# Optimization experiments

Measured on AMD Instinct MI355X. Metric: run time of the kernel, lower is better.

## Reference

```python
import jax, jax.numpy as jnp
import numpy as np

T = 0.1  # temperature (init arg t)


def setup_inputs() -> dict:
    key = jax.random.key(0)
    k0, k1, k2, k3 = jax.random.split(key, 4)
    B, C, H, W, N = 1, 64, 256, 256, 4096
    emb_0 = jax.random.normal(k0, (B, C, H, W), dtype=jnp.float32)
    emb_1 = jax.random.normal(k1, (B, C, H, W), dtype=jnp.float32)
    # module assumes embeddings are already L2-normalized along channels
    emb_0 = emb_0 / jnp.linalg.norm(emb_0, axis=1, keepdims=True)
    emb_1 = emb_1 / jnp.linalg.norm(emb_1, axis=1, keepdims=True)
    locations_0 = jax.random.randint(k2, (B, N, 2), 0, H).astype(jnp.float32)
    locations_1 = jax.random.randint(k3, (B, N, 2), 0, H).astype(jnp.float32)
    return {"emb_0": emb_0, "emb_1": emb_1,
            "locations_0": locations_0, "locations_1": locations_1}


def reference(emb_0, emb_1, locations_0, locations_1):
    b, c, H, W = emb_0.shape  # b == 1
    n = locations_0.shape[1]
    v = H * W
    # (b, v, c)
    e0 = emb_0.reshape(b, c, v).transpose(0, 2, 1)
    e1 = emb_1.reshape(b, c, v).transpose(0, 2, 1)
    # flatten 2D coords to linear indices: strides [W, 1]
    ind_kernel = jnp.array([W, 1], dtype=jnp.float32)
    ind_0 = (jnp.floor(locations_0) @ ind_kernel).astype(jnp.int32)[0]  # (n,)
    ind_1 = (jnp.floor(locations_1) @ ind_kernel).astype(jnp.int32)[0]  # (n,)
    e0 = e0[:, ind_0, :]  # (b, n, c)
    e1 = e1[:, ind_1, :]  # (b, n, c)
    emb = jnp.concatenate([e0, e1], axis=1)  # (b, 2n, c)
    sim = jnp.einsum('bic,bjc->bij', emb, emb)  # (b, 2n, 2n)
    exp = jnp.exp(sim / T)
    sum_e = jnp.sum(exp, axis=2) - np.exp(1.0 / T)  # subtract self-similarity
    u = jnp.arange(n)
    w = u + n
    e_uv = exp[:, u, w]  # (b, n) positive pairs
    loss = -jnp.sum(jnp.log(e_uv / sum_e[:, u]) + jnp.log(e_uv / sum_e[:, w]))
    return loss / (2 * n)
```

## Files before the change

kernel.cpp:

```cpp
#include <hip/hip_runtime.h>
#include <math.h>

#define HW2     65536
#define NLOC    4096
#define NROW    8192
#define CDIM    64
#define TINV    10.0f
#define EXP10   22026.465794806718f
#define NP      64
#define NPAIR   2080

#if __has_builtin(__builtin_amdgcn_exp2f)
#define ASCALE  14.426950408889634f
#define EXPFN(x) __builtin_amdgcn_exp2f(x)
#else
#define ASCALE  10.0f
#define EXPFN(x) __expf(x)
#endif

typedef __attribute__((ext_vector_type(8))) short bf16x8;
typedef __attribute__((ext_vector_type(4))) float f32x4;
typedef unsigned short u16;

__device__ __forceinline__ unsigned short f2bf(float f) {
  unsigned u = __builtin_bit_cast(unsigned, f);
  u += 0x7FFFu + ((u >> 16) & 1u);
  return (unsigned short)(u >> 16);
}
__device__ __forceinline__ float bf2f(unsigned u16v) {
  unsigned u = u16v << 16;
  return __builtin_bit_cast(float, u);
}
__device__ __forceinline__ bf16x8 scale8(bf16x8 r) {
  bf16x8 o;
#pragma unroll
  for (int j = 0; j < 8; ++j)
    o[j] = (short)f2bf(bf2f((unsigned short)r[j]) * ASCALE);
  return o;
}

__global__ __launch_bounds__(256) void gatherc_kernel(
    const float* __restrict__ emb0, const float* __restrict__ emb1,
    const float* __restrict__ loc0, const float* __restrict__ loc1,
    u16* __restrict__ Gb, unsigned* __restrict__ counter) {
  __shared__ int ind[64];
  __shared__ u16 Gs[64][18];

  const int tid   = threadIdx.x;
  const int chunk = blockIdx.x;
  const int cg    = blockIdx.y;
  const int eb    = chunk >> 6;
  const float* emb = eb ? emb1 : emb0;
  const float* loc = eb ? loc1 : loc0;

  if (chunk == 0 && cg == 0 && tid == 0) *counter = 0u;

  if (tid < 64) {
    const int u = (chunk & 63) * 64 + tid;
    float2 lv = *reinterpret_cast<const float2*>(&loc[u * 2]);
    ind[tid] = (int)floorf(lv.x) * 256 + (int)floorf(lv.y);
  }
  __syncthreads();

  const int row = tid & 63;
  const int cq  = tid >> 6;
  const int pos = ind[row];
#pragma unroll
  for (int k = 0; k < 4; ++k) {
    const int cl = cq + 4 * k;
    float v = emb[(size_t)(cg * 16 + cl) * HW2 + pos];
    Gs[row][cl] = f2bf(v);
  }
  __syncthreads();

  if (tid < 128) {
    const int r2 = tid >> 1, h = tid & 1;
    bf16x8 v = *reinterpret_cast<const bf16x8*>(&Gs[r2][h * 8]);
    *reinterpret_cast<bf16x8*>(
        &Gb[(size_t)(chunk * 64 + r2) * CDIM + cg * 16 + h * 8]) = v;
  }
}

__device__ __forceinline__ void stage_tile(u16* Bs, const u16* __restrict__ Gb,
                                           int jb, int buf, int tid, int wave,
                                           int srow, int ssl) {
#pragma unroll
  for (int r = 0; r < 2; ++r) {
    const u16* src = Gb + (size_t)(jb + r * 32 + srow) * CDIM + ssl * 8;
#if __has_builtin(__builtin_amdgcn_global_load_lds)
    u16* dst = Bs + buf * 4096 + r * 2048 + wave * 512;
    __builtin_amdgcn_global_load_lds(
        (const __attribute__((address_space(1))) unsigned int*)src,
        (__attribute__((address_space(3))) unsigned int*)dst, 16, 0, 0);
#else
    bf16x8 tmp = *reinterpret_cast<const bf16x8*>(src);
    *reinterpret_cast<bf16x8*>(Bs + buf * 4096 + r * 2048 + tid * 8) = tmp;
#endif
  }
}

__global__ __launch_bounds__(256) void simsum_tri_kernel(
    const u16* __restrict__ Gb, float* __restrict__ rowPart) {
  __shared__ u16 Bs[2 * 64 * CDIM];
  __shared__ float colRed[4][128];

  const int tid  = threadIdx.x;
  const int lane = tid & 63;
  const int wave = tid >> 6;
  const int lrow = lane & 15;
  const int kh   = lane >> 4;

  const int b = blockIdx.x;
  int p = (int)((129.0f - sqrtf(16641.0f - 8.0f * (float)b)) * 0.5f);
  if (p < 0) p = 0;
  if (p > NP - 1) p = NP - 1;
#pragma unroll
  for (int it = 0; it < 3; ++it) {
    if (p > 0 && (p * NP - p * (p - 1) / 2) > b) --p;
    else if (((p + 1) * NP - (p + 1) * p / 2) <= b) ++p;
  }
  const int q  = p + (b - (p * NP - p * (p - 1) / 2));
  const int p0 = p * 128, q0 = q * 128;
  const int i0 = p0 + wave * 32;

  const bf16x8* arowA =
      reinterpret_cast<const bf16x8*>(Gb + (size_t)(i0 + lrow) * CDIM + kh * 8);
  const bf16x8* arowB = reinterpret_cast<const bf16x8*>(
      Gb + (size_t)(i0 + 16 + lrow) * CDIM + kh * 8);
  bf16x8 aA0 = scale8(arowA[0]), aA1 = scale8(arowA[4]);
  bf16x8 aB0 = scale8(arowB[0]), aB1 = scale8(arowB[4]);

  const int srow = tid >> 3;
  const int ssl  = (tid & 7) ^ (srow & 7);
  stage_tile(Bs, Gb, q0,      0, tid, wave, srow, ssl);
  stage_tile(Bs, Gb, q0 + 64, 1, tid, wave, srow, ssl);
  __syncthreads();

  const int sp0 = ((kh ^ (lrow & 7)) << 3);
  const int sp1 = (((4 + kh) ^ (lrow & 7)) << 3);

  float accA[4][4], accB[4][4];
#pragma unroll
  for (int nf = 0; nf < 4; ++nf)
#pragma unroll
    for (int r = 0; r < 4; ++r) { accA[nf][r] = 0.f; accB[nf][r] = 0.f; }
  float colAcc[2][4];

#pragma unroll
  for (int t = 0; t < 2; ++t) {
    const u16* bs = Bs + t * 4096;
#pragma unroll
    for (int nf = 0; nf < 4; ++nf) {
      const int rb = (nf * 16 + lrow) * CDIM;
      bf16x8 b0 = *reinterpret_cast<const bf16x8*>(bs + rb + sp0);
      bf16x8 b1 = *reinterpret_cast<const bf16x8*>(bs + rb + sp1);
      f32x4 z = {0.f, 0.f, 0.f, 0.f};
      f32x4 tA = __builtin_amdgcn_mfma_f32_16x16x32_bf16(aA0, b0, z, 0, 0, 0);
      tA = __builtin_amdgcn_mfma_f32_16x16x32_bf16(aA1, b1, tA, 0, 0, 0);
      f32x4 tB = __builtin_amdgcn_mfma_f32_16x16x32_bf16(aB0, b0, z, 0, 0, 0);
      tB = __builtin_amdgcn_mfma_f32_16x16x32_bf16(aB1, b1, tB, 0, 0, 0);
      float cp = 0.f;
#pragma unroll
      for (int r = 0; r < 4; ++r) {
        float eA = EXPFN(tA[r]);
        float eB = EXPFN(tB[r]);
        accA[nf][r] += eA;
        accB[nf][r] += eB;
        cp += eA + eB;
      }
      colAcc[t][nf] = cp;
    }
  }

#pragma unroll
  for (int r = 0; r < 4; ++r) {
    float vA = (accA[0][r] + accA[1][r]) + (accA[2][r] + accA[3][r]);
    float vB = (accB[0][r] + accB[1][r]) + (accB[2][r] + accB[3][r]);
    vA += __shfl_xor(vA, 1, 16);
    vA += __shfl_xor(vA, 2, 16);
    vA += __shfl_xor(vA, 4, 16);
    vA += __shfl_xor(vA, 8, 16);
    vB += __shfl_xor(vB, 1, 16);
    vB += __shfl_xor(vB, 2, 16);
    vB += __shfl_xor(vB, 4, 16);
    vB += __shfl_xor(vB, 8, 16);
    if (lrow == 0) {
      rowPart[(size_t)(i0 + kh * 4 + r) * NP + q] = vA;
      rowPart[(size_t)(i0 + 16 + kh * 4 + r) * NP + q] = vB;
    }
  }

  if (p != q) {
#pragma unroll
    for (int t = 0; t < 2; ++t)
#pragma unroll
      for (int nf = 0; nf < 4; ++nf) {
        float c = colAcc[t][nf];
        c += __shfl_xor(c, 16, 64);
        c += __shfl_xor(c, 32, 64);
        if (kh == 0) colRed[wave][t * 64 + nf * 16 + lrow] = c;
      }
    __syncthreads();
    if (tid < 128) {
      float s = (colRed[0][tid] + colRed[1][tid]) +
                (colRed[2][tid] + colRed[3][tid]);
      rowPart[(size_t)(q0 + tid) * NP + p] = s;
    }
  }
}

__global__ __launch_bounds__(256) void finpart_kernel(
    const u16* __restrict__ Gb, const float* __restrict__ rowPart,
    float* __restrict__ partA, float* __restrict__ partB,
    unsigned* __restrict__ counter, float* __restrict__ out) {
  __shared__ float sA[256];
  __shared__ float sB[256];
  __shared__ int lastFlag;
  const int tid = threadIdx.x, b = blockIdx.x;

  float logAcc = 0.f;
  if (tid < 128) {
    const int row = b * 128 + tid;
    const float4* rp = reinterpret_cast<const float4*>(rowPart + (size_t)row * NP);
    float s = 0.f;
#pragma unroll
    for (int c = 0; c < NP / 4; ++c) {
      float4 v = rp[c];
      s += (v.x + v.y) + (v.z + v.w);
    }
    logAcc = logf(s - EXP10);
  }
  float cross = 0.f;
  if (tid < 64) {
    const int u = b * 64 + tid;
    const unsigned* r0 = reinterpret_cast<const unsigned*>(Gb + (size_t)u * CDIM);
    const unsigned* r1 =
        reinterpret_cast<const unsigned*>(Gb + (size_t)(u + NLOC) * CDIM);
#pragma unroll
    for (int c = 0; c < 32; ++c) {
      unsigned a = r0[c], bb = r1[c];
      cross += bf2f(a & 0xffffu) * bf2f(bb & 0xffffu) + bf2f(a >> 16) * bf2f(bb >> 16);
    }
  }
  sA[tid] = logAcc;
  sB[tid] = cross;
  __syncthreads();
  for (int s = 128; s > 0; s >>= 1) {
    if (tid < s) { sA[tid] += sA[tid + s]; sB[tid] += sB[tid + s]; }
    __syncthreads();
  }
  if (tid == 0) {
    __hip_atomic_store(&partA[b], sA[0], __ATOMIC_RELAXED, __HIP_MEMORY_SCOPE_AGENT);
    __hip_atomic_store(&partB[b], sB[0], __ATOMIC_RELAXED, __HIP_MEMORY_SCOPE_AGENT);
    __threadfence();
    unsigned old = atomicAdd(counter, 1u);
    lastFlag = (old == 63u) ? 1 : 0;
  }
  __syncthreads();

  if (lastFlag && tid < 64) {
    float a = __hip_atomic_load(&partA[tid], __ATOMIC_RELAXED, __HIP_MEMORY_SCOPE_AGENT);
    float c = __hip_atomic_load(&partB[tid], __ATOMIC_RELAXED, __HIP_MEMORY_SCOPE_AGENT);
#pragma unroll
    for (int s = 1; s < 64; s <<= 1) {
      a += __shfl_xor(a, s, 64);
      c += __shfl_xor(c, s, 64);
    }
    if (tid == 0) out[0] = (a - 2.0f * TINV * c) / (float)NROW;
  }
}

extern "C" void kernel_launch(void* const* d_in, const int* in_sizes, int n_in,
                              void* d_out, int out_size, void* d_ws, size_t ws_size,
                              hipStream_t stream) {
  const float* emb0 = (const float*)d_in[0];
  const float* emb1 = (const float*)d_in[1];
  const float* loc0 = (const float*)d_in[2];
  const float* loc1 = (const float*)d_in[3];
  float* out = (float*)d_out;
  char* ws = (char*)d_ws;

  u16* Gb           = (u16*)ws;
  float* rowPart    = (float*)(ws + (1ull << 20));
  float* partA      = (float*)(ws + (3ull << 20));
  float* partB      = (float*)(ws + (3ull << 20) + 256);
  unsigned* counter = (unsigned*)(ws + (3ull << 20) + 512);

  dim3 gg(128, 4);
  gatherc_kernel<<<gg, 256, 0, stream>>>(emb0, emb1, loc0, loc1, Gb, counter);
  simsum_tri_kernel<<<NPAIR, 256, 0, stream>>>(Gb, rowPart);
  finpart_kernel<<<64, 256, 0, stream>>>(Gb, rowPart, partA, partB, counter, out);
}
```

Measured before the change: 37.28 us.

## Make triangular sim kernel loop over tiles with double-buffered LDS prefetch

The similarity-sum kernel now launches a fixed 1024 blocks. Each block walks the triangular tile list with stride SBLK, and while it computes the current tile it prefetches the next tile's B operand into a second LDS buffer. The goal is to hide global-to-LDS staging latency and cut per-block launch and setup overhead. In exchange the LDS footprint doubles, which may lower occupancy. Because 2080 tiles do not divide evenly over 1024 blocks, some blocks take a third tile and leave an uneven tail.

```diff
diff --git a/kernel.cpp b/kernel.cpp
--- a/kernel.cpp
+++ b/kernel.cpp
@@ -9,6 +9,7 @@
 #define EXP10   22026.465794806718f
 #define NP      64
 #define NPAIR   2080
+#define SBLK    1024
 
 #if __has_builtin(__builtin_amdgcn_exp2f)
 #define ASCALE  14.426950408889634f
@@ -39,6 +40,19 @@
   return o;
 }
 
+__device__ __forceinline__ void tri_decode(int b, int* pOut, int* qOut) {
+  int p = (int)((129.0f - sqrtf(16641.0f - 8.0f * (float)b)) * 0.5f);
+  if (p < 0) p = 0;
+  if (p > NP - 1) p = NP - 1;
+#pragma unroll
+  for (int it = 0; it < 3; ++it) {
+    if (p > 0 && (p * NP - p * (p - 1) / 2) > b) --p;
+    else if (((p + 1) * NP - (p + 1) * p / 2) <= b) ++p;
+  }
+  *pOut = p;
+  *qOut = p + (b - (p * NP - p * (p - 1) / 2));
+}
+
 __global__ __launch_bounds__(256) void gatherc_kernel(
     const float* __restrict__ emb0, const float* __restrict__ emb1,
     const float* __restrict__ loc0, const float* __restrict__ loc1,
@@ -81,27 +95,27 @@
   }
 }
 
-__device__ __forceinline__ void stage_tile(u16* Bs, const u16* __restrict__ Gb,
-                                           int jb, int buf, int tid, int wave,
+__device__ __forceinline__ void stage_tile(u16* base, const u16* __restrict__ Gb,
+                                           int jb, int half, int tid, int wave,
                                            int srow, int ssl) {
 #pragma unroll
   for (int r = 0; r < 2; ++r) {
     const u16* src = Gb + (size_t)(jb + r * 32 + srow) * CDIM + ssl * 8;
 #if __has_builtin(__builtin_amdgcn_global_load_lds)
-    u16* dst = Bs + buf * 4096 + r * 2048 + wave * 512;
+    u16* dst = base + half * 4096 + r * 2048 + wave * 512;
     __builtin_amdgcn_global_load_lds(
         (const __attribute__((address_space(1))) unsigned int*)src,
         (__attribute__((address_space(3))) unsigned int*)dst, 16, 0, 0);
 #else
     bf16x8 tmp = *reinterpret_cast<const bf16x8*>(src);
-    *reinterpret_cast<bf16x8*>(Bs + buf * 4096 + r * 2048 + tid * 8) = tmp;
+    *reinterpret_cast<bf16x8*>(base + half * 4096 + r * 2048 + tid * 8) = tmp;
 #endif
   }
 }
 
 __global__ __launch_bounds__(256) void simsum_tri_kernel(
     const u16* __restrict__ Gb, float* __restrict__ rowPart) {
-  __shared__ u16 Bs[2 * 64 * CDIM];
+  __shared__ u16 Bs[2][2 * 64 * CDIM];
   __shared__ float colRed[4][128];
 
   const int tid  = threadIdx.x;
@@ -109,103 +123,115 @@
   const int wave = tid >> 6;
   const int lrow = lane & 15;
   const int kh   = lane >> 4;
-
-  const int b = blockIdx.x;
-  int p = (int)((129.0f - sqrtf(16641.0f - 8.0f * (float)b)) * 0.5f);
-  if (p < 0) p = 0;
-  if (p > NP - 1) p = NP - 1;
-#pragma unroll
-  for (int it = 0; it < 3; ++it) {
-    if (p > 0 && (p * NP - p * (p - 1) / 2) > b) --p;
-    else if (((p + 1) * NP - (p + 1) * p / 2) <= b) ++p;
-  }
-  const int q  = p + (b - (p * NP - p * (p - 1) / 2));
-  const int p0 = p * 128, q0 = q * 128;
-  const int i0 = p0 + wave * 32;
-
-  const bf16x8* arowA =
-      reinterpret_cast<const bf16x8*>(Gb + (size_t)(i0 + lrow) * CDIM + kh * 8);
-  const bf16x8* arowB = reinterpret_cast<const bf16x8*>(
-      Gb + (size_t)(i0 + 16 + lrow) * CDIM + kh * 8);
-  bf16x8 aA0 = scale8(arowA[0]), aA1 = scale8(arowA[4]);
-  bf16x8 aB0 = scale8(arowB[0]), aB1 = scale8(arowB[4]);
-
   const int srow = tid >> 3;
   const int ssl  = (tid & 7) ^ (srow & 7);
-  stage_tile(Bs, Gb, q0,      0, tid, wave, srow, ssl);
-  stage_tile(Bs, Gb, q0 + 64, 1, tid, wave, srow, ssl);
-  __syncthreads();
-
-  const int sp0 = ((kh ^ (lrow & 7)) << 3);
-  const int sp1 = (((4 + kh) ^ (lrow & 7)) << 3);
-
-  float accA[4][4], accB[4][4];
-#pragma unroll
-  for (int nf = 0; nf < 4; ++nf)
-#pragma unroll
-    for (int r = 0; r < 4; ++r) { accA[nf][r] = 0.f; accB[nf][r] = 0.f; }
-  float colAcc[2][4];
-
-#pragma unroll
-  for (int t = 0; t < 2; ++t) {
-    const u16* bs = Bs + t * 4096;
-#pragma unroll
-    for (int nf = 0; nf < 4; ++nf) {
-      const int rb = (nf * 16 + lrow) * CDIM;
-      bf16x8 b0 = *reinterpret_cast<const bf16x8*>(bs + rb + sp0);
-      bf16x8 b1 = *reinterpret_cast<const bf16x8*>(bs + rb + sp1);
-      f32x4 z = {0.f, 0.f, 0.f, 0.f};
-      f32x4 tA = __builtin_amdgcn_mfma_f32_16x16x32_bf16(aA0, b0, z, 0, 0, 0);
-      tA = __builtin_amdgcn_mfma_f32_16x16x32_bf16(aA1, b1, tA, 0, 0, 0);
-      f32x4 tB = __builtin_amdgcn_mfma_f32_16x16x32_bf16(aB0, b0, z, 0, 0, 0);
-      tB = __builtin_amdgcn_mfma_f32_16x16x32_bf16(aB1, b1, tB, 0, 0, 0);
-      float cp = 0.f;
-#pragma unroll
-      for (int r = 0; r < 4; ++r) {
-        float eA = EXPFN(tA[r]);
-        float eB = EXPFN(tB[r]);
-        accA[nf][r] += eA;
-        accB[nf][r] += eB;
-        cp += eA + eB;
+  const int sp0  = ((kh ^ (lrow & 7)) << 3);
+  const int sp1  = (((4 + kh) ^ (lrow & 7)) << 3);
+
+  int tile = blockIdx.x;
+  int p, q;
+  tri_decode(tile, &p, &q);
+
+  stage_tile(Bs[0], Gb, q * 128,      0, tid, wave, srow, ssl);
+  stage_tile(Bs[0], Gb, q * 128 + 64, 1, tid, wave, srow, ssl);
+  __syncthreads();
+
+  int buf = 0;
+  while (true) {
+    const int ntile = tile + SBLK;
+    int np2 = 0, nq2 = 0;
+    const bool haveNext = (ntile < NPAIR);
+    if (haveNext) {
+      tri_decode(ntile, &np2, &nq2);
+      stage_tile(Bs[buf ^ 1], Gb, nq2 * 128,      0, tid, wave, srow, ssl);
+      stage_tile(Bs[buf ^ 1], Gb, nq2 * 128 + 64, 1, tid, wave, srow, ssl);
+    }
+
+    const int p0 = p * 128, q0 = q * 128;
+    const int i0 = p0 + wave * 32;
+
+    const bf16x8* arowA = reinterpret_cast<const bf16x8*>(
+        Gb + (size_t)(i0 + lrow) * CDIM + kh * 8);
+    const bf16x8* arowB = reinterpret_cast<const bf16x8*>(
+        Gb + (size_t)(i0 + 16 + lrow) * CDIM + kh * 8);
+    bf16x8 aA0 = scale8(arowA[0]), aA1 = scale8(arowA[4]);
+    bf16x8 aB0 = scale8(arowB[0]), aB1 = scale8(arowB[4]);
+
+    float accA[4][4], accB[4][4];
+#pragma unroll
+    for (int nf = 0; nf < 4; ++nf)
+#pragma unroll
+      for (int r = 0; r < 4; ++r) { accA[nf][r] = 0.f; accB[nf][r] = 0.f; }
+    float colAcc[2][4];
+
+#pragma unroll
+    for (int t = 0; t < 2; ++t) {
+      const u16* bs = Bs[buf] + t * 4096;
+#pragma unroll
+      for (int nf = 0; nf < 4; ++nf) {
+        const int rb = (nf * 16 + lrow) * CDIM;
+        bf16x8 b0 = *reinterpret_cast<const bf16x8*>(bs + rb + sp0);
+        bf16x8 b1 = *reinterpret_cast<const bf16x8*>(bs + rb + sp1);
+        f32x4 z = {0.f, 0.f, 0.f, 0.f};
+        f32x4 tA = __builtin_amdgcn_mfma_f32_16x16x32_bf16(aA0, b0, z, 0, 0, 0);
+        tA = __builtin_amdgcn_mfma_f32_16x16x32_bf16(aA1, b1, tA, 0, 0, 0);
+        f32x4 tB = __builtin_amdgcn_mfma_f32_16x16x32_bf16(aB0, b0, z, 0, 0, 0);
+        tB = __builtin_amdgcn_mfma_f32_16x16x32_bf16(aB1, b1, tB, 0, 0, 0);
+        float cp = 0.f;
+#pragma unroll
+        for (int r = 0; r < 4; ++r) {
+          float eA = EXPFN(tA[r]);
+          float eB = EXPFN(tB[r]);
+          accA[nf][r] += eA;
+          accB[nf][r] += eB;
+          cp += eA + eB;
+        }
+        colAcc[t][nf] = cp;
       }
-      colAcc[t][nf] = cp;
-    }
-  }
-
-#pragma unroll
-  for (int r = 0; r < 4; ++r) {
-    float vA = (accA[0][r] + accA[1][r]) + (accA[2][r] + accA[3][r]);
-    float vB = (accB[0][r] + accB[1][r]) + (accB[2][r] + accB[3][r]);
-    vA += __shfl_xor(vA, 1, 16);
-    vA += __shfl_xor(vA, 2, 16);
-    vA += __shfl_xor(vA, 4, 16);
-    vA += __shfl_xor(vA, 8, 16);
-    vB += __shfl_xor(vB, 1, 16);
-    vB += __shfl_xor(vB, 2, 16);
-    vB += __shfl_xor(vB, 4, 16);
-    vB += __shfl_xor(vB, 8, 16);
-    if (lrow == 0) {
-      rowPart[(size_t)(i0 + kh * 4 + r) * NP + q] = vA;
-      rowPart[(size_t)(i0 + 16 + kh * 4 + r) * NP + q] = vB;
-    }
-  }
-
-  if (p != q) {
-#pragma unroll
-    for (int t = 0; t < 2; ++t)
-#pragma unroll
-      for (int nf = 0; nf < 4; ++nf) {
-        float c = colAcc[t][nf];
-        c += __shfl_xor(c, 16, 64);
-        c += __shfl_xor(c, 32, 64);
-        if (kh == 0) colRed[wave][t * 64 + nf * 16 + lrow] = c;
+    }
+
+#pragma unroll
+    for (int r = 0; r < 4; ++r) {
+      float vA = (accA[0][r] + accA[1][r]) + (accA[2][r] + accA[3][r]);
+      float vB = (accB[0][r] + accB[1][r]) + (accB[2][r] + accB[3][r]);
+      vA += __shfl_xor(vA, 1, 16);
+      vA += __shfl_xor(vA, 2, 16);
+      vA += __shfl_xor(vA, 4, 16);
+      vA += __shfl_xor(vA, 8, 16);
+      vB += __shfl_xor(vB, 1, 16);
+      vB += __shfl_xor(vB, 2, 16);
+      vB += __shfl_xor(vB, 4, 16);
+      vB += __shfl_xor(vB, 8, 16);
+      if (lrow == 0) {
+        rowPart[(size_t)(i0 + kh * 4 + r) * NP + q] = vA;
+        rowPart[(size_t)(i0 + 16 + kh * 4 + r) * NP + q] = vB;
       }
+    }
+
+    if (p != q) {
+#pragma unroll
+      for (int t = 0; t < 2; ++t)
+#pragma unroll
+        for (int nf = 0; nf < 4; ++nf) {
+          float c = colAcc[t][nf];
+          c += __shfl_xor(c, 16, 64);
+          c += __shfl_xor(c, 32, 64);
+          if (kh == 0) colRed[wave][t * 64 + nf * 16 + lrow] = c;
+        }
+      __syncthreads();
+      if (tid < 128) {
+        float s = (colRed[0][tid] + colRed[1][tid]) +
+                  (colRed[2][tid] + colRed[3][tid]);
+        rowPart[(size_t)(q0 + tid) * NP + p] = s;
+      }
+    }
+
     __syncthreads();
-    if (tid < 128) {
-      float s = (colRed[0][tid] + colRed[1][tid]) +
-                (colRed[2][tid] + colRed[3][tid]);
-      rowPart[(size_t)(q0 + tid) * NP + p] = s;
-    }
+    if (!haveNext) break;
+    tile = ntile;
+    p = np2;
+    q = nq2;
+    buf ^= 1;
   }
 }
 
@@ -288,6 +314,6 @@
 
   dim3 gg(128, 4);
   gatherc_kernel<<<gg, 256, 0, stream>>>(emb0, emb1, loc0, loc1, Gb, counter);
-  simsum_tri_kernel<<<NPAIR, 256, 0, stream>>>(Gb, rowPart);
+  simsum_tri_kernel<<<SBLK, 256, 0, stream>>>(Gb, rowPart);
   finpart_kernel<<<64, 256, 0, stream>>>(Gb, rowPart, partA, partB, counter, out);
 }
```

After: 43.89 us. +17.7%, slower.

## Replace scattered gather with windowed streaming read and per-window location matching

Applied to the files above, without the earlier changes.

The gather kernel now streams each 64-pixel window of all 64 channels with coalesced float4 loads, instead of issuing scattered per-element reads. Each block scans every location to find the entries that fall in its window. It then transposes the window to bf16 in shared memory and writes out the matching rows. This trades random sector reads for reading both full embedding tensors plus repeated scans of the location arrays. Entries past the 64-slot list fall back to direct scattered reads.

```diff
diff --git a/kernel.cpp b/kernel.cpp
--- a/kernel.cpp
+++ b/kernel.cpp
@@ -39,45 +39,71 @@
   return o;
 }
 
-__global__ __launch_bounds__(256) void gatherc_kernel(
+__global__ __launch_bounds__(256) void fgather_kernel(
     const float* __restrict__ emb0, const float* __restrict__ emb1,
     const float* __restrict__ loc0, const float* __restrict__ loc1,
     u16* __restrict__ Gb, unsigned* __restrict__ counter) {
-  __shared__ int ind[64];
-  __shared__ u16 Gs[64][18];
-
-  const int tid   = threadIdx.x;
-  const int chunk = blockIdx.x;
-  const int cg    = blockIdx.y;
-  const int eb    = chunk >> 6;
+  __shared__ u16 T[64 * 72];
+  __shared__ unsigned list[64];
+  __shared__ unsigned nE;
+
+  const int tid = threadIdx.x;
+  const int win = blockIdx.x;
+  const int eb  = blockIdx.y;
   const float* emb = eb ? emb1 : emb0;
   const float* loc = eb ? loc1 : loc0;
-
-  if (chunk == 0 && cg == 0 && tid == 0) *counter = 0u;
-
-  if (tid < 64) {
-    const int u = (chunk & 63) * 64 + tid;
-    float2 lv = *reinterpret_cast<const float2*>(&loc[u * 2]);
-    ind[tid] = (int)floorf(lv.x) * 256 + (int)floorf(lv.y);
-  }
-  __syncthreads();
-
-  const int row = tid & 63;
-  const int cq  = tid >> 6;
-  const int pos = ind[row];
-#pragma unroll
-  for (int k = 0; k < 4; ++k) {
-    const int cl = cq + 4 * k;
-    float v = emb[(size_t)(cg * 16 + cl) * HW2 + pos];
-    Gs[row][cl] = f2bf(v);
-  }
-  __syncthreads();
-
-  if (tid < 128) {
-    const int r2 = tid >> 1, h = tid & 1;
-    bf16x8 v = *reinterpret_cast<const bf16x8*>(&Gs[r2][h * 8]);
-    *reinterpret_cast<bf16x8*>(
-        &Gb[(size_t)(chunk * 64 + r2) * CDIM + cg * 16 + h * 8]) = v;
+  const int w0 = win * 64;
+
+  if (win == 0 && eb == 0 && tid == 0) *counter = 0u;
+  if (tid == 0) nE = 0;
+
+  const int cB = tid >> 4;
+  const int x  = tid & 15;
+  float4 v[4];
+#pragma unroll
+  for (int q = 0; q < 4; ++q)
+    v[q] = *reinterpret_cast<const float4*>(
+        &emb[(size_t)(q * 16 + cB) * HW2 + w0 + x * 4]);
+
+  __syncthreads();
+
+  for (int it = tid; it < NLOC; it += 256) {
+    float2 lv = *reinterpret_cast<const float2*>(&loc[it * 2]);
+    int ind = (int)floorf(lv.x) * 256 + (int)floorf(lv.y);
+    if ((ind >> 6) == win) {
+      unsigned slot = atomicAdd(&nE, 1u);
+      if (slot < 64u) {
+        list[slot] = ((unsigned)it << 6) | (unsigned)(ind & 63);
+      } else {
+        for (int c = 0; c < CDIM; ++c)
+          Gb[(size_t)(it + eb * NLOC) * CDIM + c] =
+              f2bf(emb[(size_t)c * HW2 + ind]);
+      }
+    }
+  }
+  __syncthreads();
+
+  const int n = (int)((nE < 64u) ? nE : 64u);
+  if (n == 0) return;
+
+#pragma unroll
+  for (int q = 0; q < 4; ++q) {
+    const int c = q * 16 + cB;
+    T[(x * 4 + 0) * 72 + c] = f2bf(v[q].x);
+    T[(x * 4 + 1) * 72 + c] = f2bf(v[q].y);
+    T[(x * 4 + 2) * 72 + c] = f2bf(v[q].z);
+    T[(x * 4 + 3) * 72 + c] = f2bf(v[q].w);
+  }
+  __syncthreads();
+
+  const int ibase = eb * NLOC;
+  const int c8 = tid & 7;
+  for (int s = (tid >> 3); s < n; s += 32) {
+    const unsigned ent = list[s];
+    const int i = (int)(ent >> 6) + ibase;
+    const int w = (int)(ent & 63u);
+    bf16x8 r = *reinterpret_cast<const bf16x8*>(&T[w * 72 + c8 * 8]);
+    *reinterpret_cast<bf16x8*>(&Gb[(size_t)i * CDIM + c8 * 8]) = r;
   }
 }
 
@@ -286,8 +312,8 @@
   float* partB      = (float*)(ws + (3ull << 20) + 256);
   unsigned* counter = (unsigned*)(ws + (3ull << 20) + 512);
 
-  dim3 gg(128, 4);
-  gatherc_kernel<<<gg, 256, 0, stream>>>(emb0, emb1, loc0, loc1, Gb, counter);
+  dim3 fg(1024, 2);
+  fgather_kernel<<<fg, 256, 0, stream>>>(emb0, emb1, loc0, loc1, Gb, counter);
   simsum_tri_kernel<<<NPAIR, 256, 0, stream>>>(Gb, rowPart);
   finpart_kernel<<<64, 256, 0, stream>>>(Gb, rowPart, partA, partB, counter, out);
 }
```

Measured after the change: 41.65 us. +11.7%, slower.
